# Kernel tuning notes

Measured on AMD Instinct MI355X. Metric: run time of the kernel, lower is better.

The kernel has to match this reference:

```python
import math
import jax, jax.numpy as jnp
import numpy as np

DIM = 2048
N_HEADS = 16
N_KV = 8
N_REP = N_HEADS // N_KV
HEAD_DIM = DIM // (2 * N_HEADS)  # 64; half-size heads per DiffAttention
L = 2048
B = 1
LAMBDA = 0.8 - 0.6 * math.exp(-0.3 * 0)  # depth=0 -> 0.2
ROPE_THETA = 10000.0


def setup_inputs() -> dict:
    key = jax.random.key(0)
    ks = jax.random.split(key, 6)
    x = jax.random.normal(ks[0], (B, L, DIM), dtype=jnp.float32)
    # RoPE tables: freqs_cis = exp(i * t * theta^(-2j/d)), stored as cos/sin
    inv_freq = 1.0 / (ROPE_THETA ** (jnp.arange(0, HEAD_DIM, 2, dtype=jnp.float32) / HEAD_DIM))
    ang = jnp.arange(L, dtype=jnp.float32)[:, None] * inv_freq[None, :]  # (L, d/2)
    cos, sin = jnp.cos(ang), jnp.sin(ang)
    scale = 0.02
    Wq = jax.random.normal(ks[1], (DIM, DIM), dtype=jnp.float32) * scale
    Wk = jax.random.normal(ks[2], (DIM, DIM // N_REP), dtype=jnp.float32) * scale
    Wv = jax.random.normal(ks[3], (DIM, DIM // N_REP), dtype=jnp.float32) * scale
    Wo = jax.random.normal(ks[4], (DIM, DIM), dtype=jnp.float32) * scale
    return {"x": x, "cos": cos, "sin": sin, "Wq": Wq, "Wk": Wk, "Wv": Wv, "Wo": Wo}


def _rope(t, cos, sin):
    # t: (B, L, H, d); rotate consecutive pairs as complex mult
    tr, ti = t[..., 0::2], t[..., 1::2]
    c = cos[None, :, None, :]
    s = sin[None, :, None, :]
    out_r = tr * c - ti * s
    out_i = tr * s + ti * c
    return jnp.stack([out_r, out_i], axis=-1).reshape(t.shape)


def reference(x, cos, sin, Wq, Wk, Wv, Wo):
    Bb, Ll, D = x.shape
    d = HEAD_DIM
    q = (x @ Wq).reshape(Bb, Ll, 2 * N_HEADS, d)
    k = (x @ Wk).reshape(Bb, Ll, 2 * N_KV, d)
    v = (x @ Wv).reshape(Bb, Ll, N_KV, 2 * d)
    q = _rope(q, cos, sin)
    k = _rope(k, cos, sin)
    # merge adjacent head pairs -> (B,H,L,2d); Q1/Q2 = the two halves
    Q = q.reshape(Bb, Ll, N_HEADS, 2 * d).transpose(0, 2, 1, 3)
    K = jnp.repeat(k.reshape(Bb, Ll, N_KV, 2 * d), N_REP, axis=2).transpose(0, 2, 1, 3)
    V = jnp.repeat(v, N_REP, axis=2).transpose(0, 2, 1, 3)  # (B,H,L,2d)
    Q1, Q2 = Q[..., :d], Q[..., d:]
    K1, K2 = K[..., :d], K[..., d:]
    scale = 1.0 / math.sqrt(d)
    causal = jnp.tril(jnp.ones((Ll, Ll), dtype=bool))

    def attn_map(Qh, Kh):
        s = jnp.einsum('bhqd,bhkd->bhqk', Qh, Kh) * scale
        s = jnp.where(causal, s, -jnp.inf)
        return jax.nn.softmax(s, axis=-1)

    attn = attn_map(Q1, K1) - LAMBDA * attn_map(Q2, K2)
    out = jnp.einsum('bhqk,bhkd->bhqd', attn, V)
    out = out.transpose(0, 2, 1, 3).reshape(Bb, Ll, D)
    return out @ Wo
```

## Files before the change

### kernel.cpp

```cpp
#include <hip/hip_runtime.h>
#include <hip/hip_bf16.h>


typedef __bf16 bf16x8 __attribute__((ext_vector_type(8)));
typedef short  s16x8  __attribute__((ext_vector_type(8)));
typedef float  f32x4  __attribute__((ext_vector_type(4)));

#define D4 4096

__device__ __forceinline__ ushort f2bfu(float f) {
  __hip_bfloat16 h = __float2bfloat16(f);
  return __builtin_bit_cast(ushort, h);
}
__device__ __forceinline__ float bfu2f(ushort u) {
  return __bfloat162float(__builtin_bit_cast(__hip_bfloat16, u));
}
__device__ __forceinline__ void gload_lds16(const void* g, void* l) {
  __builtin_amdgcn_global_load_lds(
      (const __attribute__((address_space(1))) unsigned int*)g,
      (__attribute__((address_space(3))) unsigned int*)l, 16, 0, 0);
}
__device__ __forceinline__ f32x4 mfma16(bf16x8 a, bf16x8 b, f32x4 c) {
  return __builtin_amdgcn_mfma_f32_16x16x32_bf16(a, b, c, 0, 0, 0);
}

__global__ __launch_bounds__(256) void cvt_x_kernel(const float* __restrict__ x,
                                                    ushort* __restrict__ xb) {
  const int i = blockIdx.x * 256 + threadIdx.x;
  float4 v = ((const float4*)x)[i];
  ((ushort4*)xb)[i] = make_ushort4(f2bfu(v.x), f2bfu(v.y), f2bfu(v.z), f2bfu(v.w));
}

__global__ __launch_bounds__(256) void transpose_bf16_kernel(const float* __restrict__ W,
                                                             ushort* __restrict__ WT,
                                                             int K, int N) {
  __shared__ float tile[32][33];
  const int bx = blockIdx.x, by = blockIdx.y;
  const int tx = threadIdx.x, ty = threadIdx.y;
#pragma unroll
  for (int j = 0; j < 32; j += 8)
    tile[ty + j][tx] = W[(size_t)(by * 32 + ty + j) * N + bx * 32 + tx];
  __syncthreads();
#pragma unroll
  for (int j = 0; j < 32; j += 8)
    WT[(size_t)(bx * 32 + ty + j) * K + by * 32 + tx] = f2bfu(tile[tx][ty + j]);
}

__global__ __launch_bounds__(256) void vtrans_kernel(const ushort* __restrict__ QKV,
                                                     ushort* __restrict__ VT) {
  __shared__ ushort tile[32][34];
  const int bx = blockIdx.x, by = blockIdx.y;
  const int tx = threadIdx.x, ty = threadIdx.y;
#pragma unroll
  for (int j = 0; j < 32; j += 8)
    tile[ty + j][tx] = QKV[(size_t)(bx * 32 + ty + j) * D4 + 3072 + by * 32 + tx];
  __syncthreads();
#pragma unroll
  for (int j = 0; j < 32; j += 8)
    VT[(size_t)(by * 32 + ty + j) * 2048 + bx * 32 + tx] = tile[tx][ty + j];
}

#define BM 128
#define BN 128
#define BK 64

template <int OUTF32>
__global__ __launch_bounds__(256, 2) void gemm_bt_kernel(
    const ushort* __restrict__ A, const ushort* __restrict__ B,
    float* __restrict__ Cf, ushort* __restrict__ Cb,
    int M, int N, int K) {
  __shared__ __align__(16) ushort As[BM * BK];
  __shared__ __align__(16) ushort Bs[BN * BK];
  const int tid = threadIdx.x;
  const int wv = tid >> 6, ln = tid & 63;
  const int lr = ln & 15, lh = ln >> 4;
  const int bm = blockIdx.y, bn = blockIdx.x;
  const int wr = wv >> 1, wc = wv & 1;
  const int srow = wv * 8 + (ln >> 3);
  const int scol = (ln & 7) * 8;

  f32x4 acc[4][4] = {};

  for (int k0 = 0; k0 < K; k0 += BK) {
#pragma unroll
    for (int it = 0; it < 4; ++it)
      gload_lds16(&A[(size_t)(bm * BM + it * 32 + srow) * K + k0 + scol],
                  &As[(it * 32 + wv * 8) * BK]);
#pragma unroll
    for (int it = 0; it < 4; ++it)
      gload_lds16(&B[(size_t)(bn * BN + it * 32 + srow) * K + k0 + scol],
                  &Bs[(it * 32 + wv * 8) * BK]);
    __syncthreads();
#pragma unroll
    for (int kk = 0; kk < 2; ++kk) {
      bf16x8 af[4], bfv[4];
#pragma unroll
      for (int m = 0; m < 4; ++m)
        af[m] = *(const bf16x8*)&As[(wr * 64 + m * 16 + lr) * BK + kk * 32 + lh * 8];
#pragma unroll
      for (int n = 0; n < 4; ++n)
        bfv[n] = *(const bf16x8*)&Bs[(wc * 64 + n * 16 + lr) * BK + kk * 32 + lh * 8];
#pragma unroll
      for (int m = 0; m < 4; ++m)
#pragma unroll
        for (int n = 0; n < 4; ++n)
          acc[m][n] = mfma16(af[m], bfv[n], acc[m][n]);
    }
    __syncthreads();
  }

#pragma unroll
  for (int m = 0; m < 4; ++m) {
#pragma unroll
    for (int n = 0; n < 4; ++n) {
      const int row0 = bm * BM + wr * 64 + m * 16 + lh * 4;
      const int col = bn * BN + wc * 64 + n * 16 + lr;
#pragma unroll
      for (int r = 0; r < 4; ++r) {
        if (OUTF32)
          Cf[(size_t)(row0 + r) * N + col] = acc[m][n][r];
        else
          Cb[(size_t)(row0 + r) * N + col] = f2bfu(acc[m][n][r]);
      }
    }
  }
}

__global__ __launch_bounds__(256) void rope_kernel(ushort* __restrict__ QKV,
                                                   const float* __restrict__ cosT,
                                                   const float* __restrict__ sinT) {
  const int t = blockIdx.x * 256 + threadIdx.x;
  const int l = blockIdx.y;
  const int hh = t >> 5, j = t & 31;
  const int col = (hh < 32) ? (hh * 64 + 2 * j) : (2048 + (hh - 32) * 64 + 2 * j);
  ushort* p = &QKV[(size_t)l * D4 + col];
  const float tr = bfu2f(p[0]), ti = bfu2f(p[1]);
  const float c = cosT[l * 32 + j], s = sinT[l * 32 + j];
  p[0] = f2bfu(tr * c - ti * s);
  p[1] = f2bfu(tr * s + ti * c);
}

__device__ __forceinline__ void attn_qtile(int qt, int h, int g,
                                           const ushort* __restrict__ QKV,
                                           const ushort* __restrict__ VT,
                                           ushort* __restrict__ AO,
                                           ushort* smem, int tid) {
  ushort* KsB = smem;
  ushort* Vs  = smem + 16384;
  const int wv = tid >> 6, ln = tid & 63;
  const int lr = ln & 15, lh = ln >> 4;
  const int half = wv >> 2, w4 = wv & 3;
  const int qbase = qt * 64 + w4 * 16;
  const int qh = 2 * h + half;
  ushort* Pw = smem + 24576 + wv * 1024;

  bf16x8 a[2];
#pragma unroll
  for (int kk = 0; kk < 2; ++kk)
    a[kk] = *(const bf16x8*)&QKV[(size_t)(qbase + lr) * D4 + qh * 64 + kk * 32 + lh * 8];

  f32x4 o[8] = {};
  float m[4], lsum[4];
#pragma unroll
  for (int r = 0; r < 4; ++r) { m[r] = -INFINITY; lsum[r] = 0.f; }

  auto stageK = [&](ushort* buf, int krow0) {
#pragma unroll
    for (int it = 0; it < 2; ++it) {
      const int row = it * 32 + wv * 4 + lh;
      gload_lds16(&QKV[(size_t)(krow0 + row) * D4 + 2048 + g * 128 + (lr ^ (row & 7)) * 8],
                  &buf[(it * 32 + wv * 4) * 128]);
    }
  };
  auto stageV = [&](int krow0) {
#pragma unroll
    for (int it = 0; it < 2; ++it) {
      const int dv = it * 64 + wv * 8 + (ln >> 3);
      gload_lds16(&VT[(size_t)(g * 128 + dv) * 2048 + krow0 + ((ln & 7) ^ (dv & 7)) * 8],
                  &Vs[(it * 64 + wv * 8) * 64]);
    }
  };

  stageK(KsB, 0);
  __syncthreads();

  int cur = 0;
  for (int kt = 0; kt <= qt; ++kt) {
    const int krow0 = kt * 64;
    stageV(krow0);
    if (kt < qt) stageK(KsB + (cur ^ 1) * 8192, krow0 + 64);

    const ushort* Kc = KsB + cur * 8192;
    f32x4 s[4] = {};
#pragma unroll
    for (int kk = 0; kk < 2; ++kk) {
#pragma unroll
      for (int n = 0; n < 4; ++n) {
        bf16x8 b = *(const bf16x8*)&Kc[(n * 16 + lr) * 128 +
                                       ((half << 3) + (((kk << 2) + lh) ^ (lr & 7))) * 8];
        s[n] = mfma16(a[kk], b, s[n]);
      }
    }

#pragma unroll
    for (int r = 0; r < 4; ++r) {
      const int qrow = lh * 4 + r;
      const int grow = qbase + qrow;
      float sv[4];
      float mx = -INFINITY;
#pragma unroll
      for (int n = 0; n < 4; ++n) {
        float v = s[n][r] * 0.125f;
        if (krow0 + n * 16 + lr > grow) v = -INFINITY;
        sv[n] = v;
        mx = fmaxf(mx, v);
      }
#pragma unroll
      for (int off = 1; off < 16; off <<= 1) mx = fmaxf(mx, __shfl_xor(mx, off));
      const float mnew = fmaxf(m[r], mx);
      const float alpha = __expf(m[r] - mnew);
      float sum = 0.f;
#pragma unroll
      for (int n = 0; n < 4; ++n) {
        const float p = __expf(sv[n] - mnew);
        sum += p;
        const int key = n * 16 + lr;
        Pw[qrow * 64 + (((key >> 3) ^ (qrow & 7)) << 3) + (key & 7)] = f2bfu(p);
      }
#pragma unroll
      for (int off = 1; off < 16; off <<= 1) sum += __shfl_xor(sum, off);
      lsum[r] = lsum[r] * alpha + sum;
      m[r] = mnew;
#pragma unroll
      for (int nn = 0; nn < 8; ++nn) o[nn][r] *= alpha;
    }

    if (kt < qt) asm volatile("s_waitcnt vmcnt(2)" ::: "memory");
    else         asm volatile("s_waitcnt vmcnt(0)" ::: "memory");
    __builtin_amdgcn_sched_barrier(0);
    __builtin_amdgcn_s_barrier();

#pragma unroll
    for (int kk = 0; kk < 2; ++kk) {
      bf16x8 pa = *(const bf16x8*)&Pw[lr * 64 + ((((kk << 2) + lh) ^ (lr & 7)) << 3)];
#pragma unroll
      for (int n = 0; n < 8; ++n) {
        const int dv = n * 16 + lr;
        bf16x8 bv = *(const bf16x8*)&Vs[dv * 64 + ((((kk << 2) + lh) ^ (lr & 7)) << 3)];
        o[n] = mfma16(pa, bv, o[n]);
      }
    }
    __syncthreads();
    cur ^= 1;
  }

  float* Os = (float*)smem;
  if (half == 1) {
#pragma unroll
    for (int n = 0; n < 8; ++n)
#pragma unroll
      for (int r = 0; r < 4; ++r)
        Os[(w4 * 16 + lh * 4 + r) * 128 + n * 16 + lr] = o[n][r] / lsum[r];
  }
  __syncthreads();
  if (half == 0) {
#pragma unroll
    for (int n = 0; n < 8; ++n) {
#pragma unroll
      for (int r = 0; r < 4; ++r) {
        const int grow = qbase + lh * 4 + r;
        const float v = o[n][r] / lsum[r] -
                        0.2f * Os[(w4 * 16 + lh * 4 + r) * 128 + n * 16 + lr];
        AO[(size_t)grow * 2048 + h * 128 + n * 16 + lr] = f2bfu(v);
      }
    }
  }
  __syncthreads();
}

__global__ __launch_bounds__(512, 2) void attn_kernel(const ushort* __restrict__ QKV,
                                                      const ushort* __restrict__ VT,
                                                      ushort* __restrict__ AO) {
  __shared__ __align__(16) ushort smem[32768];
  const int p = blockIdx.x, h = blockIdx.y, g = h >> 1;
  attn_qtile(p, h, g, QKV, VT, AO, smem, threadIdx.x);
  attn_qtile(31 - p, h, g, QKV, VT, AO, smem, threadIdx.x);
}

extern "C" void kernel_launch(void* const* d_in, const int* in_sizes, int n_in,
                              void* d_out, int out_size, void* d_ws, size_t ws_size,
                              hipStream_t stream) {
  (void)in_sizes; (void)n_in; (void)out_size; (void)ws_size;
  const float* x    = (const float*)d_in[0];
  const float* cosT = (const float*)d_in[1];
  const float* sinT = (const float*)d_in[2];
  const float* Wq   = (const float*)d_in[3];
  const float* Wk   = (const float*)d_in[4];
  const float* Wv   = (const float*)d_in[5];
  const float* Wo   = (const float*)d_in[6];
  float* out = (float*)d_out;

  ushort* ws = (ushort*)d_ws;
  ushort* xb   = ws;
  ushort* WT   = ws + 4194304;
  ushort* WkT  = ws + 8388608;
  ushort* WvT  = ws + 10485760;
  ushort* WoT  = ws + 12582912;
  ushort* QKVb = ws + 16777216;
  ushort* AOb  = ws + 25165824;
  ushort* VT   = ws;

  cvt_x_kernel<<<4096, 256, 0, stream>>>(x, xb);
  dim3 tb(32, 8);
  transpose_bf16_kernel<<<dim3(64, 64), tb, 0, stream>>>(Wq, WT, 2048, 2048);
  transpose_bf16_kernel<<<dim3(32, 64), tb, 0, stream>>>(Wk, WkT, 2048, 1024);
  transpose_bf16_kernel<<<dim3(32, 64), tb, 0, stream>>>(Wv, WvT, 2048, 1024);
  transpose_bf16_kernel<<<dim3(64, 64), tb, 0, stream>>>(Wo, WoT, 2048, 2048);

  gemm_bt_kernel<0><<<dim3(4096 / BN, 2048 / BM), 256, 0, stream>>>(
      xb, WT, nullptr, QKVb, 2048, 4096, 2048);

  rope_kernel<<<dim3(6, 2048), 256, 0, stream>>>(QKVb, cosT, sinT);
  vtrans_kernel<<<dim3(64, 32), tb, 0, stream>>>(QKVb, VT);

  attn_kernel<<<dim3(16, 16), 512, 0, stream>>>(QKVb, VT, AOb);

  gemm_bt_kernel<1><<<dim3(2048 / BN, 2048 / BM), 256, 0, stream>>>(
      AOb, WoT, out, nullptr, 2048, 2048, 2048);
}
```

Before: 314.3 us.

## Split attention into one q-tile per block with lazy rescale and peeled diagonal

The attention kernel now launches one block per (q-tile, head), ordered longest tiles first, instead of pairing two tiles per block. Launch bounds rise to four blocks per CU. The 1/sqrt(d) scale is folded into Q once at load. The causal mask runs only on a peeled diagonal step. Online-softmax rescaling of the accumulator is skipped when the new row max stays within a threshold of the running max. The aim is better load balance and occupancy and fewer ALU/exp ops per tile, at the cost of register pressure from the higher occupancy target and a small bf16 rounding change from pre-scaling Q.

```diff
diff --git a/kernel.cpp b/kernel.cpp
--- a/kernel.cpp
+++ b/kernel.cpp
@@ -140,14 +140,17 @@
   p[1] = f2bfu(tr * s + ti * c);
 }
 
-__device__ __forceinline__ void attn_qtile(int qt, int h, int g,
-                                           const ushort* __restrict__ QKV,
-                                           const ushort* __restrict__ VT,
-                                           ushort* __restrict__ AO,
-                                           ushort* smem, int tid) {
+__global__ __launch_bounds__(512, 4) void attn_kernel(const ushort* __restrict__ QKV,
+                                                      const ushort* __restrict__ VT,
+                                                      ushort* __restrict__ AO) {
+  __shared__ __align__(16) ushort smem[32768];
+  const int b = blockIdx.x;
+  const int qt = 31 - (b >> 4);
+  const int h = b & 15, g = h >> 1;
+
   ushort* KsB = smem;
   ushort* Vs  = smem + 16384;
-  const int wv = tid >> 6, ln = tid & 63;
+  const int tid = threadIdx.x, wv = tid >> 6, ln = tid & 63;
   const int lr = ln & 15, lh = ln >> 4;
   const int half = wv >> 2, w4 = wv & 3;
   const int qbase = qt * 64 + w4 * 16;
@@ -156,8 +159,12 @@
 
   bf16x8 a[2];
 #pragma unroll
-  for (int kk = 0; kk < 2; ++kk)
-    a[kk] = *(const bf16x8*)&QKV[(size_t)(qbase + lr) * D4 + qh * 64 + kk * 32 + lh * 8];
+  for (int kk = 0; kk < 2; ++kk) {
+    bf16x8 t = *(const bf16x8*)&QKV[(size_t)(qbase + lr) * D4 + qh * 64 + kk * 32 + lh * 8];
+#pragma unroll
+    for (int i = 0; i < 8; ++i) t[i] = (__bf16)((float)t[i] * 0.125f);
+    a[kk] = t;
+  }
 
   f32x4 o[8] = {};
   float m[4], lsum[4];
@@ -181,62 +188,80 @@
     }
   };
 
-  stageK(KsB, 0);
-  __syncthreads();
-
-  int cur = 0;
-  for (int kt = 0; kt <= qt; ++kt) {
-    const int krow0 = kt * 64;
-    stageV(krow0);
-    if (kt < qt) stageK(KsB + (cur ^ 1) * 8192, krow0 + 64);
-
-    const ushort* Kc = KsB + cur * 8192;
+  auto step = [&](int kt, bool diag, int vm_outstanding) {
+    const ushort* Kc = KsB + (kt & 1) * 8192;
     f32x4 s[4] = {};
 #pragma unroll
     for (int kk = 0; kk < 2; ++kk) {
 #pragma unroll
       for (int n = 0; n < 4; ++n) {
-        bf16x8 b = *(const bf16x8*)&Kc[(n * 16 + lr) * 128 +
-                                       ((half << 3) + (((kk << 2) + lh) ^ (lr & 7))) * 8];
-        s[n] = mfma16(a[kk], b, s[n]);
-      }
-    }
-
+        bf16x8 bb = *(const bf16x8*)&Kc[(n * 16 + lr) * 128 +
+                                        ((half << 3) + (((kk << 2) + lh) ^ (lr & 7))) * 8];
+        s[n] = mfma16(a[kk], bb, s[n]);
+      }
+    }
+
+    float sv[4][4];
+    float mx[4];
 #pragma unroll
     for (int r = 0; r < 4; ++r) {
       const int qrow = lh * 4 + r;
-      const int grow = qbase + qrow;
-      float sv[4];
-      float mx = -INFINITY;
+      float rmx = -INFINITY;
 #pragma unroll
       for (int n = 0; n < 4; ++n) {
-        float v = s[n][r] * 0.125f;
-        if (krow0 + n * 16 + lr > grow) v = -INFINITY;
-        sv[n] = v;
-        mx = fmaxf(mx, v);
-      }
-#pragma unroll
-      for (int off = 1; off < 16; off <<= 1) mx = fmaxf(mx, __shfl_xor(mx, off));
-      const float mnew = fmaxf(m[r], mx);
-      const float alpha = __expf(m[r] - mnew);
-      float sum = 0.f;
-#pragma unroll
-      for (int n = 0; n < 4; ++n) {
-        const float p = __expf(sv[n] - mnew);
-        sum += p;
-        const int key = n * 16 + lr;
-        Pw[qrow * 64 + (((key >> 3) ^ (qrow & 7)) << 3) + (key & 7)] = f2bfu(p);
-      }
-#pragma unroll
-      for (int off = 1; off < 16; off <<= 1) sum += __shfl_xor(sum, off);
-      lsum[r] = lsum[r] * alpha + sum;
-      m[r] = mnew;
-#pragma unroll
-      for (int nn = 0; nn < 8; ++nn) o[nn][r] *= alpha;
-    }
-
-    if (kt < qt) asm volatile("s_waitcnt vmcnt(2)" ::: "memory");
-    else         asm volatile("s_waitcnt vmcnt(0)" ::: "memory");
+        float v = s[n][r];
+        if (diag && (n * 16 + lr > w4 * 16 + qrow)) v = -INFINITY;
+        sv[r][n] = v;
+        rmx = fmaxf(rmx, v);
+      }
+#pragma unroll
+      for (int off = 1; off < 16; off <<= 1) rmx = fmaxf(rmx, __shfl_xor(rmx, off));
+      mx[r] = rmx;
+    }
+
+    bool small = (mx[0] <= m[0] + 8.f) && (mx[1] <= m[1] + 8.f) &&
+                 (mx[2] <= m[2] + 8.f) && (mx[3] <= m[3] + 8.f);
+    if (__all(small)) {
+#pragma unroll
+      for (int r = 0; r < 4; ++r) {
+        const int qrow = lh * 4 + r;
+        float sum = 0.f;
+#pragma unroll
+        for (int n = 0; n < 4; ++n) {
+          const float p = __expf(sv[r][n] - m[r]);
+          sum += p;
+          const int key = n * 16 + lr;
+          Pw[qrow * 64 + (((key >> 3) ^ (qrow & 7)) << 3) + (key & 7)] = f2bfu(p);
+        }
+#pragma unroll
+        for (int off = 1; off < 16; off <<= 1) sum += __shfl_xor(sum, off);
+        lsum[r] += sum;
+      }
+    } else {
+#pragma unroll
+      for (int r = 0; r < 4; ++r) {
+        const int qrow = lh * 4 + r;
+        const float mnew = fmaxf(m[r], mx[r]);
+        const float alpha = __expf(m[r] - mnew);
+        float sum = 0.f;
+#pragma unroll
+        for (int n = 0; n < 4; ++n) {
+          const float p = __expf(sv[r][n] - mnew);
+          sum += p;
+          const int key = n * 16 + lr;
+          Pw[qrow * 64 + (((key >> 3) ^ (qrow & 7)) << 3) + (key & 7)] = f2bfu(p);
+        }
+#pragma unroll
+        for (int off = 1; off < 16; off <<= 1) sum += __shfl_xor(sum, off);
+        lsum[r] = lsum[r] * alpha + sum;
+        m[r] = mnew;
+#pragma unroll
+        for (int nn = 0; nn < 8; ++nn) o[nn][r] *= alpha;
+      }
+    }
+
+    if (vm_outstanding == 2) asm volatile("s_waitcnt vmcnt(2)" ::: "memory");
+    else                     asm volatile("s_waitcnt vmcnt(0)" ::: "memory");
     __builtin_amdgcn_sched_barrier(0);
     __builtin_amdgcn_s_barrier();
 
@@ -250,9 +275,19 @@
         o[n] = mfma16(pa, bv, o[n]);
       }
     }
+  };
+
+  stageK(KsB, 0);
+  __syncthreads();
+
+  for (int kt = 0; kt < qt; ++kt) {
+    stageV(kt * 64);
+    stageK(KsB + ((kt & 1) ^ 1) * 8192, kt * 64 + 64);
+    step(kt, false, 2);
     __syncthreads();
-    cur ^= 1;
-  }
+  }
+  stageV(qt * 64);
+  step(qt, true, 0);
 
   float* Os = (float*)smem;
   if (half == 1) {
@@ -275,16 +310,6 @@
       }
     }
   }
-  __syncthreads();
-}
-
-__global__ __launch_bounds__(512, 2) void attn_kernel(const ushort* __restrict__ QKV,
-                                                      const ushort* __restrict__ VT,
-                                                      ushort* __restrict__ AO) {
-  __shared__ __align__(16) ushort smem[32768];
-  const int p = blockIdx.x, h = blockIdx.y, g = h >> 1;
-  attn_qtile(p, h, g, QKV, VT, AO, smem, threadIdx.x);
-  attn_qtile(31 - p, h, g, QKV, VT, AO, smem, threadIdx.x);
 }
 
 extern "C" void kernel_launch(void* const* d_in, const int* in_sizes, int n_in,
@@ -323,7 +348,7 @@
   rope_kernel<<<dim3(6, 2048), 256, 0, stream>>>(QKVb, cosT, sinT);
   vtrans_kernel<<<dim3(64, 32), tb, 0, stream>>>(QKVb, VT);
 
-  attn_kernel<<<dim3(16, 16), 512, 0, stream>>>(QKVb, VT, AOb);
+  attn_kernel<<<512, 512, 0, stream>>>(QKVb, VT, AOb);
 
   gemm_bt_kernel<1><<<dim3(2048 / BN, 2048 / BM), 256, 0, stream>>>(
       AOb, WoT, out, nullptr, 2048, 2048, 2048);
```

Result: slower. 364.1 us (+15.9%).
